# Kernel tuning notes

Measured on AMD Instinct MI355X. Metric: run time of the kernel, lower is better.

## Reference

```python
import jax, jax.numpy as jnp
import numpy as np

B, L, H, Z, T = 128, 4096, 1024, 256, 16  # batch, input_len(64*64), lstm_hidden, z_size, timesteps


def _lstm_cell(x, h, c, W_ih, b_ih, W_hh, b_hh):
    # PyTorch LSTMCell: gates ordered (input, forget, cell, output)
    gates = x @ W_ih.T + b_ih + h @ W_hh.T + b_hh
    i, f, g, o = jnp.split(gates, 4, axis=-1)
    c_new = jax.nn.sigmoid(f) * c + jax.nn.sigmoid(i) * jnp.tanh(g)
    h_new = jax.nn.sigmoid(o) * jnp.tanh(c_new)
    return h_new, c_new


def setup_inputs() -> dict:
    key = jax.random.key(0)
    ks = jax.random.split(key, 16)
    s = 0.02  # weight init scale
    return {
        "x": jax.random.uniform(ks[0], (B, L), dtype=jnp.float32),
        "eps": jax.random.normal(ks[1], (T, B, Z), dtype=jnp.float32),
        "c_0": jax.random.normal(ks[2], (1, L), dtype=jnp.float32),
        "h_0_enc": jax.random.normal(ks[3], (H,), dtype=jnp.float32),
        "h_0_dec": jax.random.normal(ks[4], (H,), dtype=jnp.float32),
        "W_ih_enc": jax.random.normal(ks[5], (4 * H, 2 * L + H), dtype=jnp.float32) * s,
        "b_ih_enc": jnp.zeros((4 * H,), dtype=jnp.float32),
        "W_hh_enc": jax.random.normal(ks[6], (4 * H, H), dtype=jnp.float32) * s,
        "b_hh_enc": jnp.zeros((4 * H,), dtype=jnp.float32),
        "W_mu": jax.random.normal(ks[7], (Z, H), dtype=jnp.float32) * s,
        "b_mu": jnp.zeros((Z,), dtype=jnp.float32),
        "W_sigma": jax.random.normal(ks[8], (Z, H), dtype=jnp.float32) * s,
        "b_sigma": jnp.zeros((Z,), dtype=jnp.float32),
        "W_ih_dec": jax.random.normal(ks[9], (4 * H, Z), dtype=jnp.float32) * s,
        "b_ih_dec": jnp.zeros((4 * H,), dtype=jnp.float32),
        "W_hh_dec": jax.random.normal(ks[10], (4 * H, H), dtype=jnp.float32) * s,
        "b_hh_dec": jnp.zeros((4 * H,), dtype=jnp.float32),
        "W_write": jax.random.normal(ks[11], (L, H), dtype=jnp.float32) * s,
        "b_write": jnp.zeros((L,), dtype=jnp.float32),
    }


def reference(x, eps, c_0, h_0_enc, h_0_dec,
              W_ih_enc, b_ih_enc, W_hh_enc, b_hh_enc,
              W_mu, b_mu, W_sigma, b_sigma,
              W_ih_dec, b_ih_dec, W_hh_dec, b_hh_dec,
              W_write, b_write):
    batch = x.shape[0]
    c_t = jnp.broadcast_to(c_0, (batch, L))
    h_enc = jnp.broadcast_to(h_0_enc, (batch, H))
    h_dec = jnp.broadcast_to(h_0_dec, (batch, H))
    c_enc = jnp.zeros((batch, H), dtype=x.dtype)
    c_dec = jnp.zeros((batch, H), dtype=x.dtype)

    def step(carry, eps_t):
        c_t, h_enc, c_enc, h_dec, c_dec = carry
        x_hat = x - jax.nn.sigmoid(c_t)
        r_t = jnp.concatenate((x, x_hat, h_dec), axis=-1)  # read + concat with h_dec
        h_enc, c_enc = _lstm_cell(r_t, h_enc, c_enc, W_ih_enc, b_ih_enc, W_hh_enc, b_hh_enc)
        mu = h_enc @ W_mu.T + b_mu
        logsigma = h_enc @ W_sigma.T + b_sigma
        z_t = eps_t * jnp.exp(logsigma) + mu
        h_dec, c_dec = _lstm_cell(z_t, h_dec, c_dec, W_ih_dec, b_ih_dec, W_hh_dec, b_hh_dec)
        c_t = c_t + h_dec @ W_write.T + b_write
        return (c_t, h_enc, c_enc, h_dec, c_dec), None

    (c_t, _, _, _, _), _ = jax.lax.scan(step, (c_t, h_enc, c_enc, h_dec, c_dec), eps)
    return jax.nn.sigmoid(c_t)
```

## Files before the change

kernel.cpp:

```cpp
#include <hip/hip_runtime.h>

#define B_   128
#define T_   16

typedef __bf16 bf16;
typedef __bf16 bf16x8 __attribute__((ext_vector_type(8)));
typedef float f32x4 __attribute__((ext_vector_type(4)));

#define GLL(SRC, DST) __builtin_amdgcn_global_load_lds( \
    (const __attribute__((address_space(1))) void*)(SRC), \
    (__attribute__((address_space(3))) void*)(DST), 16, 0, 0)

#define MFMA __builtin_amdgcn_mfma_f32_16x16x32_bf16
#define SLICE 524288

__device__ __forceinline__ float sigf(float x) { return 1.f / (1.f + expf(-x)); }

__device__ __forceinline__ void core64(
    bf16 (&As)[2][4096], bf16 (&Bs)[2][4096],
    const bf16* __restrict__ Ab, int lda,
    const bf16* __restrict__ Wb, int ldw,
    int nk, f32x4 (&acc)[4])
{
    const int tid = threadIdx.x, lane = tid & 63, wave = tid >> 6;
    const int srow = lane >> 3;
    const int scol = ((lane & 7) ^ srow) << 3;
    const int wr = wave & 1, wc = wave >> 1;
    const int ln = lane & 15;
    const int rA0 = wr * 32 + ln;
    const int rB0 = wc * 32 + ln;
    const int swz = (lane & 7) << 4;
    const int kq  = (lane >> 4) << 4;

    auto stage = [&](int b, int koff) {
        int c0 = wave, c1 = wave + 4;
        int ra0 = c0 * 8 + srow, ra1 = c1 * 8 + srow;
        GLL(Ab + (size_t)ra0 * lda + koff + scol, &As[b][c0 * 512]);
        GLL(Ab + (size_t)ra1 * lda + koff + scol, &As[b][c1 * 512]);
        GLL(Wb + (size_t)ra0 * ldw + koff + scol, &Bs[b][c0 * 512]);
        GLL(Wb + (size_t)ra1 * ldw + koff + scol, &Bs[b][c1 * 512]);
    };

    stage(0, 0);
    int bq = 0;
    for (int it = 0; it < nk; ++it) {
        __syncthreads();
        if (it + 1 < nk) stage(bq ^ 1, (it + 1) << 6);
        const bf16* as = As[bq];
        const bf16* bs = Bs[bq];
#pragma unroll
        for (int k2 = 0; k2 < 2; ++k2) {
            const int co = (((k2 << 6) | kq) ^ swz) >> 1;
            bf16x8 a0 = *(const bf16x8*)&as[rA0 * 64 + co];
            bf16x8 a1 = *(const bf16x8*)&as[(rA0 + 16) * 64 + co];
            bf16x8 b0 = *(const bf16x8*)&bs[rB0 * 64 + co];
            bf16x8 b1 = *(const bf16x8*)&bs[(rB0 + 16) * 64 + co];
            acc[0] = MFMA(a0, b0, acc[0], 0, 0, 0);
            acc[1] = MFMA(a0, b1, acc[1], 0, 0, 0);
            acc[2] = MFMA(a1, b0, acc[2], 0, 0, 0);
            acc[3] = MFMA(a1, b1, acc[3], 0, 0, 0);
        }
        bq ^= 1;
    }
}

__device__ __forceinline__ void store64(float* __restrict__ P, int bm, int bn,
                                        f32x4 (&acc)[4])
{
    const int lane = threadIdx.x & 63, wave = threadIdx.x >> 6;
    const int wr = wave & 1, wc = wave >> 1;
    const int ln = lane & 15, q = lane >> 4;
    const int row0 = bm + wr * 32 + q * 4;
    const int col0 = bn + wc * 32 + ln;
#pragma unroll
    for (int r = 0; r < 4; ++r) {
        P[(size_t)(row0 + r) * 4096 + col0]           = acc[0][r];
        P[(size_t)(row0 + r) * 4096 + col0 + 16]      = acc[1][r];
        P[(size_t)(row0 + 16 + r) * 4096 + col0]      = acc[2][r];
        P[(size_t)(row0 + 16 + r) * 4096 + col0 + 16] = acc[3][r];
    }
}

__global__ __launch_bounds__(256) void gemm64_k(
    const bf16* __restrict__ A, int lda,
    const bf16* __restrict__ W, int ldw, int Kc,
    float* __restrict__ P)
{
    __shared__ bf16 As[2][4096], Bs[2][4096];
    const int nt = blockIdx.x, mt = blockIdx.y, zz = blockIdx.z;
    f32x4 acc[4];
#pragma unroll
    for (int i = 0; i < 4; ++i) acc[i] = (f32x4){0.f, 0.f, 0.f, 0.f};
    const bf16* Ab = A + (size_t)mt * 64 * lda + (size_t)zz * Kc;
    const bf16* Wb = W + (size_t)nt * 64 * ldw + (size_t)zz * Kc;
    core64(As, Bs, Ab, lda, Wb, ldw, Kc >> 6, acc);
    store64(P + (size_t)zz * SLICE, mt * 64, nt * 64, acc);
}

__global__ __launch_bounds__(256) void kE_k(
    const bf16* __restrict__ hh,   const bf16* __restrict__ Wwr,
    const bf16* __restrict__ Wcat, const bf16* __restrict__ Wdh,
    float* __restrict__ wrP, float* __restrict__ encP, float* __restrict__ decP,
    int zoff)
{
    __shared__ bf16 As[2][4096], Bs[2][4096];
    const int nt = blockIdx.x, mt = blockIdx.y, zz = blockIdx.z + zoff;
    f32x4 acc[4];
#pragma unroll
    for (int i = 0; i < 4; ++i) acc[i] = (f32x4){0.f, 0.f, 0.f, 0.f};

    const bf16* Ab;
    const bf16* Wb;
    int ldw, nk;
    float* P;
    if (zz < 2) {
        Ab = hh + (size_t)mt * 64 * 2048 + zz * 512;
        Wb = Wwr + (size_t)nt * 64 * 1024 + zz * 512;
        ldw = 1024; nk = 8; P = wrP + (size_t)zz * SLICE;
    } else if (zz < 4) {
        int s = zz - 2;
        Ab = hh + (size_t)mt * 64 * 2048 + s * 1024;
        Wb = Wcat + (size_t)nt * 64 * 2048 + s * 1024;
        ldw = 2048; nk = 16; P = encP + (size_t)(4 + s) * SLICE;
    } else {
        Ab = hh + (size_t)mt * 64 * 2048;
        Wb = Wdh + (size_t)nt * 64 * 1024;
        ldw = 1024; nk = 16; P = decP + SLICE;
    }
    core64(As, Bs, Ab, 2048, Wb, ldw, nk, acc);
    store64(P, mt * 64, nt * 64, acc);
}

__global__ __launch_bounds__(256) void fin0_k(
    const float* __restrict__ P, float* __restrict__ base,
    const float* __restrict__ b1, const float* __restrict__ b2)
{
    const int i = blockIdx.x * 256 + threadIdx.x;
    const int row = i >> 10, j = i & 1023;
    const size_t off = (size_t)row * 4096 + (j << 2);
    float s0 = 0.f, s1 = 0.f, s2 = 0.f, s3 = 0.f;
#pragma unroll
    for (int z = 0; z < 4; ++z) {
        float4 p = *(const float4*)(P + (size_t)z * SLICE + off);
        s0 += p.x; s1 += p.y; s2 += p.z; s3 += p.w;
    }
    base[off + 0] = s0 + b1[j]        + b2[j];
    base[off + 1] = s1 + b1[1024 + j] + b2[1024 + j];
    base[off + 2] = s2 + b1[2048 + j] + b2[2048 + j];
    base[off + 3] = s3 + b1[3072 + j] + b2[3072 + j];
}

__global__ __launch_bounds__(256) void kB_k(
    const float* __restrict__ encP, const float* __restrict__ base,
    float* __restrict__ c_enc, bf16* __restrict__ hh)
{
    const int i = blockIdx.x * 256 + threadIdx.x;
    const int row = i >> 10, j = i & 1023;
    const size_t off = (size_t)row * 4096 + (j << 2);
    float s0 = 0.f, s1 = 0.f, s2 = 0.f, s3 = 0.f;
#pragma unroll
    for (int z = 0; z < 6; ++z) {
        float4 p = *(const float4*)(encP + (size_t)z * SLICE + off);
        s0 += p.x; s1 += p.y; s2 += p.z; s3 += p.w;
    }
    float4 bb = *(const float4*)(base + off);
    float gi = s0 + bb.x, gf = s1 + bb.y, gg = s2 + bb.z, go = s3 + bb.w;
    float cn = sigf(gf) * c_enc[i] + sigf(gi) * tanhf(gg);
    c_enc[i] = cn;
    hh[(size_t)row * 2048 + 1024 + j] = (bf16)(sigf(go) * tanhf(cn));
}

__global__ __launch_bounds__(256) void kD2_k(
    const float* __restrict__ decP,
    const float* __restrict__ b_ihd, const float* __restrict__ b_hhd,
    float* __restrict__ c_dec, bf16* __restrict__ hh)
{
    const int i = blockIdx.x * 256 + threadIdx.x;
    const int row = i >> 10, j = i & 1023;
    const size_t off = (size_t)row * 4096 + (j << 2);
    float4 p0 = *(const float4*)(decP + off);
    float4 p1 = *(const float4*)(decP + SLICE + off);
    float gi = p0.x + p1.x + b_ihd[j]        + b_hhd[j];
    float gf = p0.y + p1.y + b_ihd[1024 + j] + b_hhd[1024 + j];
    float gg = p0.z + p1.z + b_ihd[2048 + j] + b_hhd[2048 + j];
    float go = p0.w + p1.w + b_ihd[3072 + j] + b_hhd[3072 + j];
    float cn = sigf(gf) * c_dec[i] + sigf(gi) * tanhf(gg);
    c_dec[i] = cn;
    hh[(size_t)row * 2048 + j] = (bf16)(sigf(go) * tanhf(cn));
}

__global__ __launch_bounds__(256) void kF_k(
    const float* __restrict__ wrP, const float* __restrict__ b_wr,
    float* __restrict__ c_t, bf16* __restrict__ negs, float* __restrict__ outp)
{
    const int qi = blockIdx.x * 256 + threadIdx.x;
    const int row = qi >> 10, cq = qi & 1023;
    const size_t off = (size_t)row * 4096 + (cq << 2);
    float4 p0 = *(const float4*)(wrP + off);
    float4 p1 = *(const float4*)(wrP + SLICE + off);
    float4 cv = *(const float4*)(c_t + off);
    float4 bw = *(const float4*)(b_wr + (cq << 2));
    float v0 = cv.x + p0.x + p1.x + bw.x;
    float v1 = cv.y + p0.y + p1.y + bw.y;
    float v2 = cv.z + p0.z + p1.z + bw.z;
    float v3 = cv.w + p0.w + p1.w + bw.w;
    *(float4*)(c_t + off) = make_float4(v0, v1, v2, v3);
    negs[off + 0] = (bf16)(-sigf(v0));
    negs[off + 1] = (bf16)(-sigf(v1));
    negs[off + 2] = (bf16)(-sigf(v2));
    negs[off + 3] = (bf16)(-sigf(v3));
    if (outp)
        *(float4*)(outp + off) = make_float4(sigf(v0), sigf(v1), sigf(v2), sigf(v3));
}

struct SmemG32 {
    bf16 As[4][128][64];
    bf16 Ws[4][32][64];
};

__global__ __launch_bounds__(256) void kC_k(
    const bf16* __restrict__ hh, const bf16* __restrict__ Wms,
    const float* __restrict__ b_mu, const float* __restrict__ b_sig,
    const float* __restrict__ eps_t, bf16* __restrict__ zbf)
{
    __shared__ SmemG32 sm;
    const int nt = blockIdx.x;
    const int tid = threadIdx.x, lane = tid & 63, wave = tid >> 6;
    const int srow = lane >> 3, scol = ((lane & 7) ^ srow) << 3;
    const int ln = lane & 15, kq = (lane >> 4) << 4;
    const int swz = (lane & 7) << 4;
    const int rA = wave * 32 + ln;
    const bf16* Wb = Wms + (size_t)nt * 32 * 1024;
    const bf16* Ab = hh + 1024;

    f32x4 acc[2][2];
#pragma unroll
    for (int m = 0; m < 2; ++m)
#pragma unroll
        for (int n = 0; n < 2; ++n) acc[m][n] = (f32x4){0.f, 0.f, 0.f, 0.f};

    for (int it = 0; it < 4; ++it) {
        if (it) __syncthreads();
        const int koff = it * 256;
#pragma unroll
        for (int kc = 0; kc < 4; ++kc) {
            const int kg = koff + kc * 64 + scol;
#pragma unroll
            for (int i = 0; i < 4; ++i) {
                int rb = i * 32 + wave * 8;
                GLL(Ab + (size_t)(rb + srow) * 2048 + kg, &sm.As[kc][rb][0]);
            }
            GLL(Wb + (size_t)(wave * 8 + srow) * 1024 + kg, &sm.Ws[kc][wave * 8][0]);
        }
        __syncthreads();
#pragma unroll
        for (int kc = 0; kc < 4; ++kc)
#pragma unroll
            for (int k2 = 0; k2 < 2; ++k2) {
                const int co = (((k2 << 6) | kq) ^ swz) >> 1;
                bf16x8 a0 = *(const bf16x8*)&sm.As[kc][rA][co];
                bf16x8 a1 = *(const bf16x8*)&sm.As[kc][rA + 16][co];
                bf16x8 b0 = *(const bf16x8*)&sm.Ws[kc][ln][co];
                bf16x8 b1 = *(const bf16x8*)&sm.Ws[kc][ln + 16][co];
                acc[0][0] = MFMA(a0, b0, acc[0][0], 0, 0, 0);
                acc[0][1] = MFMA(a0, b1, acc[0][1], 0, 0, 0);
                acc[1][0] = MFMA(a1, b0, acc[1][0], 0, 0, 0);
                acc[1][1] = MFMA(a1, b1, acc[1][1], 0, 0, 0);
            }
    }
    __syncthreads();

    float* Cl = (float*)&sm;
    const int q = lane >> 4;
#pragma unroll
    for (int f = 0; f < 2; ++f)
#pragma unroll
        for (int n = 0; n < 2; ++n)
#pragma unroll
            for (int r = 0; r < 4; ++r)
                Cl[(wave * 32 + f * 16 + q * 4 + r) * 33 + n * 16 + ln] = acc[f][n][r];
    __syncthreads();

#pragma unroll
    for (int it = 0; it < 8; ++it) {
        int li = it * 256 + tid;
        int row = li >> 4, zl = li & 15;
        int zi = nt * 16 + zl;
        float mu = Cl[row * 33 + zl * 2]     + b_mu[zi];
        float ls = Cl[row * 33 + zl * 2 + 1] + b_sig[zi];
        float z = eps_t[row * 256 + zi] * expf(ls) + mu;
        zbf[(size_t)row * 256 + zi] = (bf16)z;
    }
}

#define PBL (B_ * 4096)
#define PBH (B_ * 1024)

__global__ void init_k(const float* __restrict__ x, const float* __restrict__ c0,
                       const float* __restrict__ h0e, const float* __restrict__ h0d,
                       float* __restrict__ c_t, float* __restrict__ c_enc,
                       float* __restrict__ c_dec, bf16* __restrict__ negs,
                       bf16* __restrict__ hh, bf16* __restrict__ x_bf) {
    int i = blockIdx.x * 256 + threadIdx.x;
    if (i >= PBL) return;
    int n = i & 4095;
    float c = c0[n];
    c_t[i] = c;
    negs[i] = (bf16)(-sigf(c));
    x_bf[i] = (bf16)x[i];
    if (i < PBH) {
        int row = i >> 10, j = i & 1023;
        c_enc[i] = 0.f;
        c_dec[i] = 0.f;
        hh[(size_t)row * 2048 + j]        = (bf16)h0d[j];
        hh[(size_t)row * 2048 + 1024 + j] = (bf16)h0e[j];
    }
}

__device__ __forceinline__ bf16x8 cvt8(const float* s) {
    float4 a = *(const float4*)s, b = *(const float4*)(s + 4);
    bf16x8 v = { (bf16)a.x, (bf16)a.y, (bf16)a.z, (bf16)a.w,
                 (bf16)b.x, (bf16)b.y, (bf16)b.z, (bf16)b.w };
    return v;
}

__global__ void conv_es_k(const float* __restrict__ Wih, const float* __restrict__ Whh,
                          bf16* __restrict__ wxh, bf16* __restrict__ wsum,
                          bf16* __restrict__ wcat) {
    int id = blockIdx.x * 256 + threadIdx.x;
    if (id >= 4096 * 768) return;
    int np = id / 768, c = (id - np * 768) * 8;
    int n = ((np & 3) << 10) + (np >> 2);
    if (c < 4096) {
        const float* sx = Wih + (size_t)n * 9216 + c;
        const float* sh = sx + 4096;
        float4 a = *(const float4*)sh, b = *(const float4*)(sh + 4);
        float4 e = *(const float4*)sx, f = *(const float4*)(sx + 4);
        bf16x8 vh = { (bf16)a.x, (bf16)a.y, (bf16)a.z, (bf16)a.w,
                      (bf16)b.x, (bf16)b.y, (bf16)b.z, (bf16)b.w };
        bf16x8 vs = { (bf16)(a.x + e.x), (bf16)(a.y + e.y), (bf16)(a.z + e.z), (bf16)(a.w + e.w),
                      (bf16)(b.x + f.x), (bf16)(b.y + f.y), (bf16)(b.z + f.z), (bf16)(b.w + f.w) };
        *(bf16x8*)(wxh  + (size_t)np * 4096 + c) = vh;
        *(bf16x8*)(wsum + (size_t)np * 4096 + c) = vs;
    } else if (c < 5120) {
        *(bf16x8*)(wcat + (size_t)np * 2048 + (c - 4096)) =
            cvt8(Wih + (size_t)n * 9216 + 8192 + (c - 4096));
    } else {
        *(bf16x8*)(wcat + (size_t)np * 2048 + 1024 + (c - 5120)) =
            cvt8(Whh + (size_t)n * 1024 + (c - 5120));
    }
}

__global__ void conv_dec_k(const float* __restrict__ Wih, const float* __restrict__ Whh,
                           bf16* __restrict__ wdz, bf16* __restrict__ wdh) {
    int id = blockIdx.x * 256 + threadIdx.x;
    if (id >= 4096 * 160) return;
    int np = id / 160, c = (id - np * 160) * 8;
    int n = ((np & 3) << 10) + (np >> 2);
    if (c < 256)
        *(bf16x8*)(wdz + (size_t)np * 256 + c) = cvt8(Wih + (size_t)n * 256 + c);
    else
        *(bf16x8*)(wdh + (size_t)np * 1024 + (c - 256)) =
            cvt8(Whh + (size_t)n * 1024 + (c - 256));
}

__global__ void conv_ms_k(const float* __restrict__ Wmu, const float* __restrict__ Wsig,
                          bf16* __restrict__ dst) {
    int id = blockIdx.x * 256 + threadIdx.x;
    if (id >= 512 * 128) return;
    int np = id >> 7, c = (id & 127) * 8;
    int zi = np >> 1;
    const float* src = ((np & 1) ? Wsig : Wmu) + (size_t)zi * 1024 + c;
    *(bf16x8*)(dst + (size_t)np * 1024 + c) = cvt8(src);
}

__global__ void conv_wr_k(const float* __restrict__ Wwr, bf16* __restrict__ dst) {
    int id = blockIdx.x * 256 + threadIdx.x;
    if (id >= 4096 * 128) return;
    *(bf16x8*)(dst + (size_t)id * 8) = cvt8(Wwr + (size_t)id * 8);
}

extern "C" void kernel_launch(void* const* d_in, const int* in_sizes, int n_in,
                              void* d_out, int out_size, void* d_ws, size_t ws_size,
                              hipStream_t stream) {
    const float* x      = (const float*)d_in[0];
    const float* eps    = (const float*)d_in[1];
    const float* c0     = (const float*)d_in[2];
    const float* h0e    = (const float*)d_in[3];
    const float* h0d    = (const float*)d_in[4];
    const float* W_ih_e = (const float*)d_in[5];
    const float* b_ih_e = (const float*)d_in[6];
    const float* W_hh_e = (const float*)d_in[7];
    const float* b_hh_e = (const float*)d_in[8];
    const float* W_mu   = (const float*)d_in[9];
    const float* b_mu   = (const float*)d_in[10];
    const float* W_sig  = (const float*)d_in[11];
    const float* b_sig  = (const float*)d_in[12];
    const float* W_ih_d = (const float*)d_in[13];
    const float* b_ih_d = (const float*)d_in[14];
    const float* W_hh_d = (const float*)d_in[15];
    const float* b_hh_d = (const float*)d_in[16];
    const float* W_wr   = (const float*)d_in[17];
    const float* b_wr   = (const float*)d_in[18];
    float* out = (float*)d_out;

    float* f = (float*)d_ws;
    float* c_t   = f; f += SLICE;
    float* base  = f; f += SLICE;
    float* encP  = f; f += (size_t)6 * SLICE;
    float* decP  = f; f += (size_t)2 * SLICE;
    float* wrP   = f; f += (size_t)2 * SLICE;
    float* c_enc = f; f += 131072;
    float* c_dec = f; f += 131072;
    bf16* bp    = (bf16*)f;
    bf16* negs  = bp; bp += (size_t)B_ * 4096;
    bf16* hh    = bp; bp += (size_t)B_ * 2048;
    bf16* zbf   = bp; bp += (size_t)B_ * 256;
    bf16* x_bf  = bp; bp += (size_t)B_ * 4096;
    bf16* Wxh   = bp; bp += (size_t)4096 * 4096;
    bf16* Wsum  = bp; bp += (size_t)4096 * 4096;
    bf16* Wcat  = bp; bp += (size_t)4096 * 2048;
    bf16* Wdz   = bp; bp += (size_t)4096 * 256;
    bf16* Wdh   = bp; bp += (size_t)4096 * 1024;
    bf16* Wms   = bp; bp += (size_t)512 * 1024;
    bf16* Wwr   = bp; bp += (size_t)4096 * 1024;

    dim3 blk(256);

    init_k<<<(PBL + 255) / 256, blk, 0, stream>>>(x, c0, h0e, h0d, c_t, c_enc, c_dec,
                                                  negs, hh, x_bf);
    conv_es_k<<<(4096 * 768 + 255) / 256, blk, 0, stream>>>(W_ih_e, W_hh_e,
                                                            Wxh, Wsum, Wcat);
    conv_dec_k<<<(4096 * 160 + 255) / 256, blk, 0, stream>>>(W_ih_d, W_hh_d, Wdz, Wdh);
    conv_ms_k<<<(512 * 128 + 255) / 256, blk, 0, stream>>>(W_mu, W_sig, Wms);
    conv_wr_k<<<(4096 * 128 + 255) / 256, blk, 0, stream>>>(W_wr, Wwr);

    gemm64_k<<<dim3(64, 2, 4), blk, 0, stream>>>(x_bf, 4096, Wsum, 4096, 1024, encP);
    fin0_k<<<dim3(512), blk, 0, stream>>>(encP, base, b_ih_e, b_hh_e);

    kE_k<<<dim3(64, 2, 3), blk, 0, stream>>>(hh, Wwr, Wcat, Wdh, wrP, encP, decP, 2);

    for (int t = 0; t < T_; ++t) {
        gemm64_k<<<dim3(64, 2, 4), blk, 0, stream>>>(negs, 4096, Wxh, 4096, 1024, encP);
        kB_k<<<dim3(512), blk, 0, stream>>>(encP, base, c_enc, hh);
        kC_k<<<dim3(16), blk, 0, stream>>>(hh, Wms, b_mu, b_sig,
                                           eps + (size_t)t * (B_ * 256), zbf);
        gemm64_k<<<dim3(64, 2, 1), blk, 0, stream>>>(zbf, 256, Wdz, 256, 256, decP);
        kD2_k<<<dim3(512), blk, 0, stream>>>(decP, b_ih_d, b_hh_d, c_dec, hh);
        kE_k<<<dim3(64, 2, 5), blk, 0, stream>>>(hh, Wwr, Wcat, Wdh, wrP, encP, decP, 0);
        kF_k<<<dim3(512), blk, 0, stream>>>(wrP, b_wr, c_t, negs,
                                            (t == T_ - 1) ? out : nullptr);
    }
}
```

Before: 921.1 us.

## Split-K wider with bf16 partials and fuse decoder z-GEMM into LSTM cell

Splits the per-step GEMMs into more K-slices (8 for the x_hat GEMM, 8 z-slices in kE), doubling the number of blocks so more CUs are busy. Partial sums are now stored as bf16 instead of fp32, halving partial-buffer traffic. The decoder input GEMM (z @ Wdz) is fused with the decoder LSTM cell into a single kernel, removing one launch and one round-trip of partials. The cost is reduced accuracy from summing bf16-rounded partials, and more partial slices for the cell kernels to read.

```diff
diff --git a/kernel.cpp b/kernel.cpp
--- a/kernel.cpp
+++ b/kernel.cpp
@@ -4,6 +4,7 @@
 #define T_   16
 
 typedef __bf16 bf16;
+typedef __bf16 bf16x4 __attribute__((ext_vector_type(4)));
 typedef __bf16 bf16x8 __attribute__((ext_vector_type(8)));
 typedef float f32x4 __attribute__((ext_vector_type(4)));
 
@@ -64,8 +65,8 @@
     }
 }
 
-__device__ __forceinline__ void store64(float* __restrict__ P, int bm, int bn,
-                                        f32x4 (&acc)[4])
+__device__ __forceinline__ void store64f(float* __restrict__ P, int bm, int bn,
+                                         f32x4 (&acc)[4])
 {
     const int lane = threadIdx.x & 63, wave = threadIdx.x >> 6;
     const int wr = wave & 1, wc = wave >> 1;
@@ -81,6 +82,23 @@
     }
 }
 
+__device__ __forceinline__ void store64b(bf16* __restrict__ P, int bm, int bn,
+                                         f32x4 (&acc)[4])
+{
+    const int lane = threadIdx.x & 63, wave = threadIdx.x >> 6;
+    const int wr = wave & 1, wc = wave >> 1;
+    const int ln = lane & 15, q = lane >> 4;
+    const int row0 = bm + wr * 32 + q * 4;
+    const int col0 = bn + wc * 32 + ln;
+#pragma unroll
+    for (int r = 0; r < 4; ++r) {
+        P[(size_t)(row0 + r) * 4096 + col0]           = (bf16)acc[0][r];
+        P[(size_t)(row0 + r) * 4096 + col0 + 16]      = (bf16)acc[1][r];
+        P[(size_t)(row0 + 16 + r) * 4096 + col0]      = (bf16)acc[2][r];
+        P[(size_t)(row0 + 16 + r) * 4096 + col0 + 16] = (bf16)acc[3][r];
+    }
+}
+
 __global__ __launch_bounds__(256) void gemm64_k(
     const bf16* __restrict__ A, int lda,
     const bf16* __restrict__ W, int ldw, int Kc,
@@ -94,13 +112,29 @@
     const bf16* Ab = A + (size_t)mt * 64 * lda + (size_t)zz * Kc;
     const bf16* Wb = W + (size_t)nt * 64 * ldw + (size_t)zz * Kc;
     core64(As, Bs, Ab, lda, Wb, ldw, Kc >> 6, acc);
-    store64(P + (size_t)zz * SLICE, mt * 64, nt * 64, acc);
+    store64f(P + (size_t)zz * SLICE, mt * 64, nt * 64, acc);
+}
+
+__global__ __launch_bounds__(256) void gemm64b_k(
+    const bf16* __restrict__ A, int lda,
+    const bf16* __restrict__ W, int ldw, int Kc,
+    bf16* __restrict__ P)
+{
+    __shared__ bf16 As[2][4096], Bs[2][4096];
+    const int nt = blockIdx.x, mt = blockIdx.y, zz = blockIdx.z;
+    f32x4 acc[4];
+#pragma unroll
+    for (int i = 0; i < 4; ++i) acc[i] = (f32x4){0.f, 0.f, 0.f, 0.f};
+    const bf16* Ab = A + (size_t)mt * 64 * lda + (size_t)zz * Kc;
+    const bf16* Wb = W + (size_t)nt * 64 * ldw + (size_t)zz * Kc;
+    core64(As, Bs, Ab, lda, Wb, ldw, Kc >> 6, acc);
+    store64b(P + (size_t)zz * SLICE, mt * 64, nt * 64, acc);
 }
 
 __global__ __launch_bounds__(256) void kE_k(
     const bf16* __restrict__ hh,   const bf16* __restrict__ Wwr,
     const bf16* __restrict__ Wcat, const bf16* __restrict__ Wdh,
-    float* __restrict__ wrP, float* __restrict__ encP, float* __restrict__ decP,
+    bf16* __restrict__ wrP, bf16* __restrict__ encP, bf16* __restrict__ decP,
     int zoff)
 {
     __shared__ bf16 As[2][4096], Bs[2][4096];
@@ -111,24 +145,25 @@
 
     const bf16* Ab;
     const bf16* Wb;
-    int ldw, nk;
-    float* P;
+    int ldw;
+    bf16* P;
     if (zz < 2) {
         Ab = hh + (size_t)mt * 64 * 2048 + zz * 512;
         Wb = Wwr + (size_t)nt * 64 * 1024 + zz * 512;
-        ldw = 1024; nk = 8; P = wrP + (size_t)zz * SLICE;
-    } else if (zz < 4) {
+        ldw = 1024; P = wrP + (size_t)zz * SLICE;
+    } else if (zz < 6) {
         int s = zz - 2;
-        Ab = hh + (size_t)mt * 64 * 2048 + s * 1024;
-        Wb = Wcat + (size_t)nt * 64 * 2048 + s * 1024;
-        ldw = 2048; nk = 16; P = encP + (size_t)(4 + s) * SLICE;
+        Ab = hh + (size_t)mt * 64 * 2048 + s * 512;
+        Wb = Wcat + (size_t)nt * 64 * 2048 + s * 512;
+        ldw = 2048; P = encP + (size_t)(8 + s) * SLICE;
     } else {
-        Ab = hh + (size_t)mt * 64 * 2048;
-        Wb = Wdh + (size_t)nt * 64 * 1024;
-        ldw = 1024; nk = 16; P = decP + SLICE;
-    }
-    core64(As, Bs, Ab, 2048, Wb, ldw, nk, acc);
-    store64(P, mt * 64, nt * 64, acc);
+        int g = zz - 6;
+        Ab = hh + (size_t)mt * 64 * 2048 + g * 512;
+        Wb = Wdh + (size_t)nt * 64 * 1024 + g * 512;
+        ldw = 1024; P = decP + (size_t)g * SLICE;
+    }
+    core64(As, Bs, Ab, 2048, Wb, ldw, 8, acc);
+    store64b(P, mt * 64, nt * 64, acc);
 }
 
 __global__ __launch_bounds__(256) void fin0_k(
@@ -151,7 +186,7 @@
 }
 
 __global__ __launch_bounds__(256) void kB_k(
-    const float* __restrict__ encP, const float* __restrict__ base,
+    const bf16* __restrict__ encP, const float* __restrict__ base,
     float* __restrict__ c_enc, bf16* __restrict__ hh)
 {
     const int i = blockIdx.x * 256 + threadIdx.x;
@@ -159,9 +194,9 @@
     const size_t off = (size_t)row * 4096 + (j << 2);
     float s0 = 0.f, s1 = 0.f, s2 = 0.f, s3 = 0.f;
 #pragma unroll
-    for (int z = 0; z < 6; ++z) {
-        float4 p = *(const float4*)(encP + (size_t)z * SLICE + off);
-        s0 += p.x; s1 += p.y; s2 += p.z; s3 += p.w;
+    for (int z = 0; z < 12; ++z) {
+        bf16x4 p = *(const bf16x4*)(encP + (size_t)z * SLICE + off);
+        s0 += (float)p[0]; s1 += (float)p[1]; s2 += (float)p[2]; s3 += (float)p[3];
     }
     float4 bb = *(const float4*)(base + off);
     float gi = s0 + bb.x, gf = s1 + bb.y, gg = s2 + bb.z, go = s3 + bb.w;
@@ -170,40 +205,21 @@
     hh[(size_t)row * 2048 + 1024 + j] = (bf16)(sigf(go) * tanhf(cn));
 }
 
-__global__ __launch_bounds__(256) void kD2_k(
-    const float* __restrict__ decP,
-    const float* __restrict__ b_ihd, const float* __restrict__ b_hhd,
-    float* __restrict__ c_dec, bf16* __restrict__ hh)
-{
-    const int i = blockIdx.x * 256 + threadIdx.x;
-    const int row = i >> 10, j = i & 1023;
-    const size_t off = (size_t)row * 4096 + (j << 2);
-    float4 p0 = *(const float4*)(decP + off);
-    float4 p1 = *(const float4*)(decP + SLICE + off);
-    float gi = p0.x + p1.x + b_ihd[j]        + b_hhd[j];
-    float gf = p0.y + p1.y + b_ihd[1024 + j] + b_hhd[1024 + j];
-    float gg = p0.z + p1.z + b_ihd[2048 + j] + b_hhd[2048 + j];
-    float go = p0.w + p1.w + b_ihd[3072 + j] + b_hhd[3072 + j];
-    float cn = sigf(gf) * c_dec[i] + sigf(gi) * tanhf(gg);
-    c_dec[i] = cn;
-    hh[(size_t)row * 2048 + j] = (bf16)(sigf(go) * tanhf(cn));
-}
-
 __global__ __launch_bounds__(256) void kF_k(
-    const float* __restrict__ wrP, const float* __restrict__ b_wr,
+    const bf16* __restrict__ wrP, const float* __restrict__ b_wr,
     float* __restrict__ c_t, bf16* __restrict__ negs, float* __restrict__ outp)
 {
     const int qi = blockIdx.x * 256 + threadIdx.x;
     const int row = qi >> 10, cq = qi & 1023;
     const size_t off = (size_t)row * 4096 + (cq << 2);
-    float4 p0 = *(const float4*)(wrP + off);
-    float4 p1 = *(const float4*)(wrP + SLICE + off);
+    bf16x4 p0 = *(const bf16x4*)(wrP + off);
+    bf16x4 p1 = *(const bf16x4*)(wrP + SLICE + off);
     float4 cv = *(const float4*)(c_t + off);
     float4 bw = *(const float4*)(b_wr + (cq << 2));
-    float v0 = cv.x + p0.x + p1.x + bw.x;
-    float v1 = cv.y + p0.y + p1.y + bw.y;
-    float v2 = cv.z + p0.z + p1.z + bw.z;
-    float v3 = cv.w + p0.w + p1.w + bw.w;
+    float v0 = cv.x + (float)p0[0] + (float)p1[0] + bw.x;
+    float v1 = cv.y + (float)p0[1] + (float)p1[1] + bw.y;
+    float v2 = cv.z + (float)p0[2] + (float)p1[2] + bw.z;
+    float v3 = cv.w + (float)p0[3] + (float)p1[3] + bw.w;
     *(float4*)(c_t + off) = make_float4(v0, v1, v2, v3);
     negs[off + 0] = (bf16)(-sigf(v0));
     negs[off + 1] = (bf16)(-sigf(v1));
@@ -290,6 +306,94 @@
         float ls = Cl[row * 33 + zl * 2 + 1] + b_sig[zi];
         float z = eps_t[row * 256 + zi] * expf(ls) + mu;
         zbf[(size_t)row * 256 + zi] = (bf16)z;
+    }
+}
+
+struct SmemD {
+    bf16 As[4][128][64];
+    bf16 Ws[4][64][64];
+};
+
+__global__ __launch_bounds__(256) void kD_k(
+    const bf16* __restrict__ zbf, const bf16* __restrict__ Wdz,
+    const bf16* __restrict__ decP,
+    const float* __restrict__ b_ihd, const float* __restrict__ b_hhd,
+    float* __restrict__ c_dec, bf16* __restrict__ hh)
+{
+    __shared__ SmemD sm;
+    const int nt = blockIdx.x;
+    const int tid = threadIdx.x, lane = tid & 63, wave = tid >> 6;
+    const int srow = lane >> 3, scol = ((lane & 7) ^ srow) << 3;
+    const int ln = lane & 15, q = lane >> 4;
+    const int kq = q << 4, swz = (lane & 7) << 4;
+    const int wr = wave & 1, wc = wave >> 1;
+    const bf16* Wb = Wdz + (size_t)nt * 64 * 256;
+
+    f32x4 acc[4][2];
+#pragma unroll
+    for (int f = 0; f < 4; ++f)
+#pragma unroll
+        for (int n = 0; n < 2; ++n) acc[f][n] = (f32x4){0.f, 0.f, 0.f, 0.f};
+
+#pragma unroll
+    for (int kc = 0; kc < 4; ++kc) {
+        const int kg = kc * 64 + scol;
+#pragma unroll
+        for (int i = 0; i < 4; ++i) {
+            int rb = i * 32 + wave * 8;
+            GLL(zbf + (size_t)(rb + srow) * 256 + kg, &sm.As[kc][rb][0]);
+        }
+#pragma unroll
+        for (int i = 0; i < 2; ++i) {
+            int rbw = i * 32 + wave * 8;
+            GLL(Wb + (size_t)(rbw + srow) * 256 + kg, &sm.Ws[kc][rbw][0]);
+        }
+    }
+    __syncthreads();
+#pragma unroll
+    for (int kc = 0; kc < 4; ++kc)
+#pragma unroll
+        for (int k2 = 0; k2 < 2; ++k2) {
+            const int co = (((k2 << 6) | kq) ^ swz) >> 1;
+            bf16x8 b0 = *(const bf16x8*)&sm.Ws[kc][wc * 32 + ln][co];
+            bf16x8 b1 = *(const bf16x8*)&sm.Ws[kc][wc * 32 + ln + 16][co];
+#pragma unroll
+            for (int f = 0; f < 4; ++f) {
+                bf16x8 a = *(const bf16x8*)&sm.As[kc][wr * 64 + f * 16 + ln][co];
+                acc[f][0] = MFMA(a, b0, acc[f][0], 0, 0, 0);
+                acc[f][1] = MFMA(a, b1, acc[f][1], 0, 0, 0);
+            }
+        }
+    __syncthreads();
+
+    float* Cl = (float*)&sm;
+#pragma unroll
+    for (int f = 0; f < 4; ++f)
+#pragma unroll
+        for (int n = 0; n < 2; ++n)
+#pragma unroll
+            for (int r = 0; r < 4; ++r)
+                Cl[(wr * 64 + f * 16 + q * 4 + r) * 66 + wc * 32 + n * 16 + ln] = acc[f][n][r];
+    __syncthreads();
+
+#pragma unroll
+    for (int it = 0; it < 8; ++it) {
+        int li = it * 256 + tid;
+        int row = li >> 4, jl = li & 15;
+        int J = nt * 16 + jl;
+        const float* cr = &Cl[row * 66 + jl * 4];
+        int gcol = nt * 64 + jl * 4;
+        const bf16* gp = decP + (size_t)row * 4096 + gcol;
+        bf16x4 g0v = *(const bf16x4*)gp;
+        bf16x4 g1v = *(const bf16x4*)(gp + SLICE);
+        float gi = cr[0] + (float)g0v[0] + (float)g1v[0] + b_ihd[J]        + b_hhd[J];
+        float gf = cr[1] + (float)g0v[1] + (float)g1v[1] + b_ihd[1024 + J] + b_hhd[1024 + J];
+        float gg = cr[2] + (float)g0v[2] + (float)g1v[2] + b_ihd[2048 + J] + b_hhd[2048 + J];
+        float go = cr[3] + (float)g0v[3] + (float)g1v[3] + b_ihd[3072 + J] + b_hhd[3072 + J];
+        int ci = row * 1024 + J;
+        float cn = sigf(gf) * c_dec[ci] + sigf(gi) * tanhf(gg);
+        c_dec[ci] = cn;
+        hh[(size_t)row * 2048 + J] = (bf16)(sigf(go) * tanhf(cn));
     }
 }
 
@@ -407,12 +511,13 @@
     float* f = (float*)d_ws;
     float* c_t   = f; f += SLICE;
     float* base  = f; f += SLICE;
-    float* encP  = f; f += (size_t)6 * SLICE;
-    float* decP  = f; f += (size_t)2 * SLICE;
-    float* wrP   = f; f += (size_t)2 * SLICE;
+    float* pP    = f; f += (size_t)4 * SLICE;
     float* c_enc = f; f += 131072;
     float* c_dec = f; f += 131072;
     bf16* bp    = (bf16*)f;
+    bf16* encP  = bp; bp += (size_t)12 * SLICE;
+    bf16* decP  = bp; bp += (size_t)2 * SLICE;
+    bf16* wrP   = bp; bp += (size_t)2 * SLICE;
     bf16* negs  = bp; bp += (size_t)B_ * 4096;
     bf16* hh    = bp; bp += (size_t)B_ * 2048;
     bf16* zbf   = bp; bp += (size_t)B_ * 256;
@@ -435,19 +540,18 @@
     conv_ms_k<<<(512 * 128 + 255) / 256, blk, 0, stream>>>(W_mu, W_sig, Wms);
     conv_wr_k<<<(4096 * 128 + 255) / 256, blk, 0, stream>>>(W_wr, Wwr);
 
-    gemm64_k<<<dim3(64, 2, 4), blk, 0, stream>>>(x_bf, 4096, Wsum, 4096, 1024, encP);
-    fin0_k<<<dim3(512), blk, 0, stream>>>(encP, base, b_ih_e, b_hh_e);
-
-    kE_k<<<dim3(64, 2, 3), blk, 0, stream>>>(hh, Wwr, Wcat, Wdh, wrP, encP, decP, 2);
+    gemm64_k<<<dim3(64, 2, 4), blk, 0, stream>>>(x_bf, 4096, Wsum, 4096, 1024, pP);
+    fin0_k<<<dim3(512), blk, 0, stream>>>(pP, base, b_ih_e, b_hh_e);
+
+    kE_k<<<dim3(64, 2, 6), blk, 0, stream>>>(hh, Wwr, Wcat, Wdh, wrP, encP, decP, 2);
 
     for (int t = 0; t < T_; ++t) {
-        gemm64_k<<<dim3(64, 2, 4), blk, 0, stream>>>(negs, 4096, Wxh, 4096, 1024, encP);
+        gemm64b_k<<<dim3(64, 2, 8), blk, 0, stream>>>(negs, 4096, Wxh, 4096, 512, encP);
         kB_k<<<dim3(512), blk, 0, stream>>>(encP, base, c_enc, hh);
         kC_k<<<dim3(16), blk, 0, stream>>>(hh, Wms, b_mu, b_sig,
                                            eps + (size_t)t * (B_ * 256), zbf);
-        gemm64_k<<<dim3(64, 2, 1), blk, 0, stream>>>(zbf, 256, Wdz, 256, 256, decP);
-        kD2_k<<<dim3(512), blk, 0, stream>>>(decP, b_ih_d, b_hh_d, c_dec, hh);
-        kE_k<<<dim3(64, 2, 5), blk, 0, stream>>>(hh, Wwr, Wcat, Wdh, wrP, encP, decP, 0);
+        kD_k<<<dim3(64), blk, 0, stream>>>(zbf, Wdz, decP, b_ih_d, b_hh_d, c_dec, hh);
+        kE_k<<<dim3(64, 2, 8), blk, 0, stream>>>(hh, Wwr, Wcat, Wdh, wrP, encP, decP, 0);
         kF_k<<<dim3(512), blk, 0, stream>>>(wrP, b_wr, c_t, negs,
                                             (t == T_ - 1) ? out : nullptr);
     }
```

Result: faster. 840.6 us, median of 2 (-8.7%).
